# Kernel optimization log

Hardware: AMD Instinct MI355X
Metric: run time of the kernel (lower is better)

## Reference

```python
import jax, jax.numpy as jnp
import numpy as np

N_NODES = 100000
N_EDGES = 1600000
IN_FEATS = 256
OUT_FEATS = 128
GAMMA = 1.0


def setup_inputs() -> dict:
    key = jax.random.key(0)
    k1, k2, k3, k4, k5 = jax.random.split(key, 5)
    glorot = np.sqrt(6.0 / (IN_FEATS + OUT_FEATS)).astype(np.float32)
    feat = jax.random.normal(k1, (N_NODES, IN_FEATS), dtype=jnp.float32)
    W_mean = jax.random.uniform(k2, (IN_FEATS, OUT_FEATS), dtype=jnp.float32, minval=-glorot, maxval=glorot)
    W_var = jax.random.uniform(k3, (IN_FEATS, OUT_FEATS), dtype=jnp.float32, minval=-glorot, maxval=glorot)
    src = jax.random.randint(k4, (N_EDGES,), 0, N_NODES, dtype=jnp.int64 if jax.config.jax_enable_x64 else jnp.int32)
    dst = jax.random.randint(k5, (N_EDGES,), 0, N_NODES, dtype=jnp.int64 if jax.config.jax_enable_x64 else jnp.int32)
    return {"feat": feat, "W_mean": W_mean, "W_var": W_var, "src": src, "dst": dst}


def reference(feat, W_mean, W_var, src, dst):
    # dense projections + relu (no bias, as bias=False)
    mean = jax.nn.relu(jnp.matmul(feat, W_mean))   # [N, F]
    var = jax.nn.relu(jnp.matmul(feat, W_var))     # [N, F]
    attention = jnp.exp(-GAMMA * var)
    # in-degrees from dst edge endpoints, clamped to >= 1
    degs = jax.ops.segment_sum(jnp.ones_like(dst, dtype=jnp.float32), dst, num_segments=N_NODES)
    degs = jnp.clip(degs, 1.0)
    norm1 = (degs ** -0.5)[:, None]                # [N, 1] = D^{-1/2}
    norm2 = norm1 * norm1                          # [N, 1] = D^{-1}
    m_msg = mean * attention * norm1
    v_msg = var * attention * attention * norm2
    # copy_src + sum aggregation (SpMM over edge list)
    mean_agg = jax.ops.segment_sum(m_msg[src], dst, num_segments=N_NODES) * norm1
    var_agg = jax.ops.segment_sum(v_msg[src], dst, num_segments=N_NODES) * norm2
    return mean_agg, var_agg
```

## Files before the change

### kernel.cpp

```cpp
#include <hip/hip_runtime.h>
#include <hip/hip_bf16.h>

#define N_NODES 100000
#define N_EDGES 1600000
#define OUTF 128
#define INF 256
#define SCAN_CHUNK 1024
#define SCAN_BLOCKS 98
#define M_TILES 6250

typedef _Float16 f16;
typedef _Float16 half8 __attribute__((ext_vector_type(8)));
typedef _Float16 half4 __attribute__((ext_vector_type(4)));
typedef _Float16 half2v __attribute__((ext_vector_type(2)));
typedef float floatx4 __attribute__((ext_vector_type(4)));

__global__ void count_rank_kernel(const int* __restrict__ dst, int E,
                                  int* __restrict__ deg, int* __restrict__ rank) {
    int i = blockIdx.x * blockDim.x + threadIdx.x;
    if (i < E) rank[i] = atomicAdd(&deg[dst[i]], 1);
}

__global__ __launch_bounds__(256) void scan_partial_kernel(const int* __restrict__ deg, int n,
                                                           int* __restrict__ partial) {
    __shared__ int red[256];
    int b = blockIdx.x, t = threadIdx.x;
    int base = b * SCAN_CHUNK;
    int s = 0;
    for (int i = t; i < SCAN_CHUNK; i += 256) {
        int idx = base + i;
        if (idx < n) s += deg[idx];
    }
    red[t] = s;
    __syncthreads();
    for (int off = 128; off > 0; off >>= 1) {
        if (t < off) red[t] += red[t + off];
        __syncthreads();
    }
    if (t == 0) partial[b] = red[0];
}

__global__ __launch_bounds__(128) void scan_top_kernel(int* __restrict__ partial, int nb,
                                                       int* __restrict__ row_start, int n) {
    __shared__ int sc[128];
    int t = threadIdx.x;
    int v = (t < nb) ? partial[t] : 0;
    sc[t] = v;
    __syncthreads();
    for (int off = 1; off < 128; off <<= 1) {
        int val = sc[t];
        int add = (t >= off) ? sc[t - off] : 0;
        __syncthreads();
        sc[t] = val + add;
        __syncthreads();
    }
    if (t < nb) partial[t] = sc[t] - v;
    if (t == 127) row_start[n] = sc[127];
}

__global__ __launch_bounds__(256) void scan_final_kernel(const int* __restrict__ deg, int n,
                                                         const int* __restrict__ partial,
                                                         int* __restrict__ row_start,
                                                         float* __restrict__ norm1,
                                                         float* __restrict__ norm2) {
    __shared__ int sc[256];
    int b = blockIdx.x, t = threadIdx.x;
    int base = b * SCAN_CHUNK + t * 4;
    int v[4];
    int tsum = 0;
#pragma unroll
    for (int j = 0; j < 4; j++) {
        int idx = base + j;
        v[j] = (idx < n) ? deg[idx] : 0;
        tsum += v[j];
    }
    sc[t] = tsum;
    __syncthreads();
    for (int off = 1; off < 256; off <<= 1) {
        int val = sc[t];
        int add = (t >= off) ? sc[t - off] : 0;
        __syncthreads();
        sc[t] = val + add;
        __syncthreads();
    }
    int run = sc[t] - tsum + partial[b];
#pragma unroll
    for (int j = 0; j < 4; j++) {
        int idx = base + j;
        if (idx < n) {
            row_start[idx] = run;
            float d = (float)(v[j] > 0 ? v[j] : 1);
            norm1[idx] = rsqrtf(d);
            norm2[idx] = 1.0f / d;
            run += v[j];
        }
    }
}

__global__ void scatter_edges_kernel(const int* __restrict__ src, const int* __restrict__ dst,
                                     const int* __restrict__ rank,
                                     const int* __restrict__ row_start,
                                     int E, int* __restrict__ srcs_sorted) {
    int i = blockIdx.x * blockDim.x + threadIdx.x;
    if (i < E) {
        srcs_sorted[row_start[dst[i]] + rank[i]] = src[i];
    }
}

__global__ __launch_bounds__(256) void convert_B_kernel(const float* __restrict__ Wm,
                                                        const float* __restrict__ Wv,
                                                        f16* __restrict__ Bt) {
    int k = threadIdx.x;
    int ng = blockIdx.x;
    int g = ng >> 4, i = ng & 15;
    int ch = g >> 3, w = (g >> 1) & 3, cg = g & 1;
    int col = ch * 64 + w * 16 + i;
    const float* srcW = cg ? Wv : Wm;
    Bt[ng * 256 + k] = (f16)srcW[k * 128 + col];
}

__global__ __launch_bounds__(256, 3) void proj_mfma_kernel(const float* __restrict__ feat,
                                                           const f16* __restrict__ Bt,
                                                           const float* __restrict__ norm1,
                                                           const float* __restrict__ norm2,
                                                           f16* __restrict__ msg) {
    int tid = threadIdx.x;
    int w = tid >> 6;
    int lane = tid & 63;
    int quad = lane >> 4;
    int l15 = lane & 15;
    int ch = blockIdx.x & 1;
    int tbase = blockIdx.x >> 1;

    half8 b[2][8];
#pragma unroll
    for (int cg = 0; cg < 2; cg++) {
        int g = ch * 8 + w * 2 + cg;
        const f16* bp = Bt + (size_t)(g * 16 + l15) * 256 + quad * 8;
#pragma unroll
        for (int kf = 0; kf < 8; kf++) {
            b[cg][kf] = *(const half8*)(bp + kf * 32);
        }
    }

    int col = ch * 64 + w * 16 + l15;

    for (int t = tbase; t < M_TILES; t += 1250) {
        int m0 = t * 16;
        half8 a[8];
        const float* ap = feat + (size_t)(m0 + l15) * 256 + quad * 8;
#pragma unroll
        for (int kf = 0; kf < 8; kf++) {
            floatx4 f0 = *(const floatx4*)(ap + kf * 32);
            floatx4 f1 = *(const floatx4*)(ap + kf * 32 + 4);
            half8 h;
            h[0] = (f16)f0.x; h[1] = (f16)f0.y; h[2] = (f16)f0.z; h[3] = (f16)f0.w;
            h[4] = (f16)f1.x; h[5] = (f16)f1.y; h[6] = (f16)f1.z; h[7] = (f16)f1.w;
            a[kf] = h;
        }

        float s1r[4], s2r[4];
#pragma unroll
        for (int r = 0; r < 4; r++) {
            int node = m0 + quad * 4 + r;
            s1r[r] = norm1[node];
            s2r[r] = norm2[node];
        }

        floatx4 acc0 = (floatx4){0.f, 0.f, 0.f, 0.f};
        floatx4 acc1 = (floatx4){0.f, 0.f, 0.f, 0.f};
#pragma unroll
        for (int kf = 0; kf < 8; kf++) {
            acc0 = __builtin_amdgcn_mfma_f32_16x16x32_f16(a[kf], b[0][kf], acc0, 0, 0, 0);
            acc1 = __builtin_amdgcn_mfma_f32_16x16x32_f16(a[kf], b[1][kf], acc1, 0, 0, 0);
        }

#pragma unroll
        for (int r = 0; r < 4; r++) {
            int node = m0 + quad * 4 + r;
            float m = fmaxf(acc0[r], 0.f);
            float v = fmaxf(acc1[r], 0.f);
            float att = __expf(-v);
            half2v pr;
            pr[0] = (f16)(m * att * s1r[r]);
            pr[1] = (f16)(v * att * att * s2r[r]);
            *(half2v*)(msg + (size_t)node * 256 + col * 2) = pr;
        }
    }
}

__global__ __launch_bounds__(256) void agg_kernel(const int* __restrict__ row_start,
                                                  const int* __restrict__ srcs,
                                                  const f16* __restrict__ msg,
                                                  const float* __restrict__ norm1,
                                                  const float* __restrict__ norm2,
                                                  float* __restrict__ out_mean,
                                                  float* __restrict__ out_var) {
    int d = blockIdx.x * 4 + (threadIdx.x >> 6);
    int lane = threadIdx.x & 63;
    int s0 = row_start[d];
    int s1 = row_start[d + 1];
    float am0 = 0.f, am1 = 0.f, av0 = 0.f, av1 = 0.f;
    int i = s0;
    for (; i + 7 < s1; i += 8) {
        half4 h[8];
#pragma unroll
        for (int j = 0; j < 8; j++) {
            h[j] = *(const half4*)(msg + (size_t)srcs[i + j] * 256 + lane * 4);
        }
#pragma unroll
        for (int j = 0; j < 8; j++) {
            am0 += (float)h[j][0];
            av0 += (float)h[j][1];
            am1 += (float)h[j][2];
            av1 += (float)h[j][3];
        }
    }
    for (; i < s1; i++) {
        half4 ha = *(const half4*)(msg + (size_t)srcs[i] * 256 + lane * 4);
        am0 += (float)ha[0];
        av0 += (float)ha[1];
        am1 += (float)ha[2];
        av1 += (float)ha[3];
    }
    float k1 = norm1[d], k2 = norm2[d];
    float2 om = make_float2(am0 * k1, am1 * k1);
    float2 ov = make_float2(av0 * k2, av1 * k2);
    *(float2*)(out_mean + (size_t)d * 128 + lane * 2) = om;
    *(float2*)(out_var + (size_t)d * 128 + lane * 2) = ov;
}

extern "C" void kernel_launch(void* const* d_in, const int* in_sizes, int n_in,
                              void* d_out, int out_size, void* d_ws, size_t ws_size,
                              hipStream_t stream) {
    const float* feat = (const float*)d_in[0];
    const float* Wm = (const float*)d_in[1];
    const float* Wv = (const float*)d_in[2];
    const int* src = (const int*)d_in[3];
    const int* dst = (const int*)d_in[4];
    float* out = (float*)d_out;

    const int N = N_NODES;
    const int E = N_EDGES;

    char* wsp = (char*)d_ws;
    auto carve = [&](size_t bytes) {
        char* p = wsp;
        wsp += (bytes + 255) & ~(size_t)255;
        return p;
    };
    f16* msg = (f16*)carve((size_t)N * 256 * sizeof(f16));
    f16* Bt = (f16*)carve((size_t)256 * 256 * sizeof(f16));
    int* srcs_sorted = (int*)carve((size_t)E * 4);
    int* rank = (int*)carve((size_t)E * 4);
    int* deg = (int*)carve((size_t)N * 4);
    int* row_start = (int*)carve((size_t)(N + 1) * 4);
    float* norm1 = (float*)carve((size_t)N * 4);
    float* norm2 = (float*)carve((size_t)N * 4);
    int* partial = (int*)carve(128 * 4);

    hipMemsetAsync(deg, 0, (size_t)N * 4, stream);

    count_rank_kernel<<<(E + 255) / 256, 256, 0, stream>>>(dst, E, deg, rank);
    convert_B_kernel<<<256, 256, 0, stream>>>(Wm, Wv, Bt);
    scan_partial_kernel<<<SCAN_BLOCKS, 256, 0, stream>>>(deg, N, partial);
    scan_top_kernel<<<1, 128, 0, stream>>>(partial, SCAN_BLOCKS, row_start, N);
    scan_final_kernel<<<SCAN_BLOCKS, 256, 0, stream>>>(deg, N, partial, row_start, norm1, norm2);
    scatter_edges_kernel<<<(E + 255) / 256, 256, 0, stream>>>(src, dst, rank, row_start, E,
                                                              srcs_sorted);
    proj_mfma_kernel<<<2500, 256, 0, stream>>>(feat, Bt, norm1, norm2, msg);
    agg_kernel<<<N / 4, 256, 0, stream>>>(row_start, srcs_sorted, msg, norm1, norm2,
                                          out, out + (size_t)N * OUTF);
}
```

Baseline: 491.8 us.

## Double-buffer feat tiles into LDS with async global_load_lds in projection

The projection kernel now stages each 16-row fp32 feat tile into a double-buffered, XOR-swizzled shared-memory buffer using async global-to-LDS loads. The next tile's load is issued before the current tile is converted and run through MFMA. This is meant to hide global memory latency in the dense projection. In exchange it uses 32KB of LDS per block, adds a barrier per tile, and pins the B fragments in registers with empty asm statements. The projection is only one stage of the pipeline, so the effect on total time is bounded by its share.

```diff
diff --git a/kernel.cpp b/kernel.cpp
--- a/kernel.cpp
+++ b/kernel.cpp
@@ -124,6 +124,8 @@
                                                            const float* __restrict__ norm1,
                                                            const float* __restrict__ norm2,
                                                            f16* __restrict__ msg) {
+    __shared__ float As[2][16 * 256];
+
     int tid = threadIdx.x;
     int w = tid >> 6;
     int lane = tid & 63;
@@ -142,23 +144,58 @@
             b[cg][kf] = *(const half8*)(bp + kf * 32);
         }
     }
+#pragma unroll
+    for (int cg = 0; cg < 2; cg++) {
+#pragma unroll
+        for (int kf = 0; kf < 8; kf++) {
+            asm volatile("" : "+v"(b[cg][kf]));
+        }
+    }
 
     int col = ch * 64 + w * 16 + l15;
 
+    int swz = (l15 & 7) << 4;
+    int rb0 = l15 * 1024 + ((quad * 32) ^ swz);
+    int rb1 = l15 * 1024 + ((quad * 32 + 16) ^ swz);
+
+    int lsw = lane * 16;
+
+    auto stage = [&](int buf, int t) {
+        int m0 = t * 16;
+#pragma unroll
+        for (int j = 0; j < 4; j++) {
+            int r = w * 4 + j;
+            const char* gp = (const char*)(feat + (size_t)(m0 + r) * 256)
+                             + (lsw ^ ((r & 7) << 4));
+            char* lp = (char*)&As[buf][0] + r * 1024;
+            __builtin_amdgcn_global_load_lds(
+                (const __attribute__((address_space(1))) void*)gp,
+                (__attribute__((address_space(3))) void*)lp, 16, 0, 0);
+        }
+    };
+
+    stage(0, tbase);
+    int cur = 0;
+
     for (int t = tbase; t < M_TILES; t += 1250) {
-        int m0 = t * 16;
+        __syncthreads();
+
+        int tn = t + 1250;
+        if (tn < M_TILES) stage(cur ^ 1, tn);
+
+        const char* ab = (const char*)&As[cur][0];
         half8 a[8];
-        const float* ap = feat + (size_t)(m0 + l15) * 256 + quad * 8;
 #pragma unroll
         for (int kf = 0; kf < 8; kf++) {
-            floatx4 f0 = *(const floatx4*)(ap + kf * 32);
-            floatx4 f1 = *(const floatx4*)(ap + kf * 32 + 4);
+            floatx4 f0 = *(const floatx4*)(ab + rb0 + kf * 128);
+            floatx4 f1 = *(const floatx4*)(ab + rb1 + kf * 128);
             half8 h;
             h[0] = (f16)f0.x; h[1] = (f16)f0.y; h[2] = (f16)f0.z; h[3] = (f16)f0.w;
             h[4] = (f16)f1.x; h[5] = (f16)f1.y; h[6] = (f16)f1.z; h[7] = (f16)f1.w;
             a[kf] = h;
         }
 
+        int m0 = t * 16;
         float s1r[4], s2r[4];
 #pragma unroll
         for (int r = 0; r < 4; r++) {
@@ -186,6 +223,7 @@
             pr[1] = (f16)(v * att * att * s2r[r]);
             *(half2v*)(msg + (size_t)node * 256 + col * 2) = pr;
         }
+        cur ^= 1;
     }
 }
 
```

New measurement: 434.9 us. -11.6%, faster.
